# Kernel tuning notes

Measured on AMD Instinct MI355X. Metric: run time of the kernel, lower is better.

The kernel has to match this reference:

```python
import jax, jax.numpy as jnp
import numpy as np

NUM_HEADS = 16

def setup_inputs() -> dict:
    key = jax.random.key(0)
    ks = jax.random.split(key, 6)
    C = 512
    nW, B, N = 64, 4, 144
    x = jax.random.normal(ks[0], (B * nW, N, C), dtype=jnp.float32)
    mask = jax.random.randint(ks[1], (nW, N, N), 0, 2, dtype=jnp.int32)
    Wqkv = jax.random.normal(ks[2], (C, 3 * C), dtype=jnp.float32) * (1.0 / np.sqrt(C))
    bqkv = jnp.zeros((3 * C,), dtype=jnp.float32)
    Wproj = jax.random.normal(ks[3], (C, C), dtype=jnp.float32) * (1.0 / np.sqrt(C))
    bproj = jnp.zeros((C,), dtype=jnp.float32)
    return {"x": x, "mask": mask, "Wqkv": Wqkv, "bqkv": bqkv, "Wproj": Wproj, "bproj": bproj}

def reference(x, mask, Wqkv, bqkv, Wproj, bproj):
    Bn, N, C = x.shape
    H = NUM_HEADS
    D = C // H
    nW = mask.shape[0]
    B = Bn // nW
    scale = 1.0 / jnp.sqrt(jnp.asarray(D, dtype=x.dtype))

    qkv = x @ Wqkv + bqkv                        # (Bn, N, 3C)
    qkv = qkv.reshape(Bn, N, 3, H, D)            # packed order (qkv, H, D)
    qkv = jnp.transpose(qkv, (2, 0, 3, 1, 4))    # (3, Bn, H, N, D)
    q, k, v = qkv[0], qkv[1], qkv[2]

    # split window-batch dim: (B nW) -> B, nW
    q = q.reshape(B, nW, H, N, D)
    k = k.reshape(B, nW, H, N, D)
    v = v.reshape(B, nW, H, N, D)

    attn = jnp.einsum('bwhnd,bwhmd->bwhnm', q, k) * scale
    bias = jnp.where(mask == 0, -jnp.inf, 0.0).astype(x.dtype)  # (nW, N, N)
    attn = attn + bias.reshape(1, nW, 1, N, N)
    attn = jax.nn.softmax(attn, axis=-1)

    out = jnp.einsum('bwhnm,bwhmd->bwhnd', attn, v)   # (B, nW, H, N, D)
    out = jnp.transpose(out, (0, 1, 3, 2, 4)).reshape(Bn, N, C)
    return out @ Wproj + bproj
```

## Files before the change

kernel.cpp:

```cpp
#include <hip/hip_runtime.h>

typedef unsigned short u16;
typedef unsigned int u32;
typedef __attribute__((ext_vector_type(4))) float f32x4;
typedef __attribute__((ext_vector_type(8))) short bf16x8;
typedef __attribute__((ext_vector_type(4))) u32 u32x4;

__device__ __forceinline__ u16 f2bf(float f) {
  union { float f; u32 u; } v; v.f = f;
  u32 r = v.u + 0x7fffu + ((v.u >> 16) & 1u);
  return (u16)(r >> 16);
}

__device__ __forceinline__ u16 f2bf_rne(float f) {
  u32 w;
  asm("v_cvt_pk_bf16_f32 %0, %1, %2" : "=v"(w) : "v"(f), "v"(f));
  return (u16)w;
}

__device__ __forceinline__ void gload_lds16(const u16* g, u16* l) {
  __builtin_amdgcn_global_load_lds((__attribute__((address_space(1))) const void*)g,
                                   (__attribute__((address_space(3))) void*)l,
                                   16, 0, 0);
}

__global__ void __launch_bounds__(256) k_transpose_w(const float* __restrict__ W,
                                                     u16* __restrict__ Wt, int K, int Nc) {
  __shared__ u16 t[64][72];
  const int tid = threadIdx.x;
  const int kb = blockIdx.x * 64, nb = blockIdx.y * 64;
  const int c4 = (tid & 15) * 4;
  const int r0 = tid >> 4;
#pragma unroll
  for (int rr = 0; rr < 4; ++rr) {
    int r = rr * 16 + r0;
    float4 v = *(const float4*)(W + (size_t)(kb + r) * Nc + nb + c4);
    t[r][c4 + 0] = f2bf(v.x);
    t[r][c4 + 1] = f2bf(v.y);
    t[r][c4 + 2] = f2bf(v.z);
    t[r][c4 + 3] = f2bf(v.w);
  }
  __syncthreads();
  const int c8 = (tid & 7) * 8;
  const int rn = tid >> 3;
#pragma unroll
  for (int rr = 0; rr < 2; ++rr) {
    int n = rr * 32 + rn;
    u16 tmp[8];
#pragma unroll
    for (int j = 0; j < 8; ++j) tmp[j] = t[c8 + j][n];
    *(u32x4*)(Wt + (size_t)(nb + n) * K + kb + c8) = *(const u32x4*)tmp;
  }
}

__global__ void k_mask_bits(const int* __restrict__ mask, u32* __restrict__ mtab) {
  int idx = blockIdx.x * blockDim.x + threadIdx.x;
  if (idx >= 64 * 144 * 8) return;
  int wd = idx & 7;
  int r = idx >> 3;
  u32 bits = 0;
  if (wd < 5) {
    int base = r * 144 + wd * 32;
    int nmax = 144 - wd * 32;
    if (nmax > 32) nmax = 32;
    for (int b = 0; b < nmax; ++b) bits |= (mask[base + b] ? 1u : 0u) << b;
  }
  mtab[idx] = bits;
}

template <bool OUT_BF16, bool A_FP32>
__global__ void __launch_bounds__(256, 3) k_gemm(const void* __restrict__ Ap,
                                                 const u16* __restrict__ Bt,
                                                 const float* __restrict__ bias,
                                                 void* __restrict__ D,
                                                 int Nc, int K, int NB) {
  __shared__ u16 As[128 * 68];
  __shared__ u16 Bs[2][128 * 64];
  const int tid = threadIdx.x;
  const int wave = tid >> 6, lane = tid & 63;
  const int wr = wave >> 1, wc = wave & 1;
  const int l15 = lane & 15, g = lane >> 4;
  const int sx = l15 & 7;
  const f32x4 fzero = {0.f, 0.f, 0.f, 0.f};

  const int cpx = gridDim.x >> 3;
  const int swz = (blockIdx.x & 7) * cpx + (blockIdx.x >> 3);
  const int bm = swz / NB, bn = swz % NB;

  const u16* Bb = Bt + (size_t)bn * 128 * K;

  int rr[4], cc[4];
#pragma unroll
  for (int i = 0; i < 4; ++i) {
    int e = i * 256 + tid;
    rr[i] = e >> 3;
    cc[i] = e & 7;
  }

  f32x4 acc[4][4];
#pragma unroll
  for (int m = 0; m < 4; ++m)
#pragma unroll
    for (int n = 0; n < 4; ++n) acc[m][n] = fzero;

  f32x4 areg[8];
  u32x4 aregb[4];

  auto A_LOAD = [&](int ks) {
    if constexpr (A_FP32) {
      const float* Af = (const float*)Ap;
#pragma unroll
      for (int i = 0; i < 4; ++i) {
        const float* p = Af + (size_t)(bm * 128 + rr[i]) * K + ks + cc[i] * 8;
        areg[2 * i] = *(const f32x4*)(p);
        areg[2 * i + 1] = *(const f32x4*)(p + 4);
      }
    } else {
      const u16* Ab = (const u16*)Ap + (size_t)bm * 128 * K;
#pragma unroll
      for (int i = 0; i < 4; ++i)
        aregb[i] = *(const u32x4*)(Ab + (size_t)rr[i] * K + ks + cc[i] * 8);
    }
  };

  auto A_WRITE = [&]() {
#pragma unroll
    for (int i = 0; i < 4; ++i) {
      u32x4 wv;
      if constexpr (A_FP32) {
        u32 w0, w1, w2, w3;
        asm("v_cvt_pk_bf16_f32 %0, %1, %2" : "=v"(w0) : "v"(areg[2 * i][0]), "v"(areg[2 * i][1]));
        asm("v_cvt_pk_bf16_f32 %0, %1, %2" : "=v"(w1) : "v"(areg[2 * i][2]), "v"(areg[2 * i][3]));
        asm("v_cvt_pk_bf16_f32 %0, %1, %2" : "=v"(w2) : "v"(areg[2 * i + 1][0]), "v"(areg[2 * i + 1][1]));
        asm("v_cvt_pk_bf16_f32 %0, %1, %2" : "=v"(w3) : "v"(areg[2 * i + 1][2]), "v"(areg[2 * i + 1][3]));
        wv[0] = w0; wv[1] = w1; wv[2] = w2; wv[3] = w3;
      } else {
        wv = aregb[i];
      }
      *(u32x4*)(&As[rr[i] * 68 + cc[i] * 8]) = wv;
    }
  };

  auto B_STAGE = [&](int buf, int ks) {
#pragma unroll
    for (int i = 0; i < 4; ++i) {
      int cs = cc[i] ^ (rr[i] & 7);
      gload_lds16(Bb + (size_t)rr[i] * K + ks + (cs << 3), &Bs[buf][(i * 256 + tid) * 8]);
    }
  };

  auto COMPUTE = [&](int buf) {
#pragma unroll
    for (int kk = 0; kk < 2; ++kk) {
      bf16x8 a[4], b[4];
#pragma unroll
      for (int m = 0; m < 4; ++m)
        a[m] = *(const bf16x8*)(&As[(wr * 64 + m * 16 + l15) * 68 + (kk * 4 + g) * 8]);
#pragma unroll
      for (int n = 0; n < 4; ++n)
        b[n] = *(const bf16x8*)(&Bs[buf][(wc * 64 + n * 16 + l15) * 64 + (((kk * 4 + g) ^ sx) << 3)]);
#pragma unroll
      for (int m = 0; m < 4; ++m)
#pragma unroll
        for (int n = 0; n < 4; ++n)
          acc[m][n] = __builtin_amdgcn_mfma_f32_16x16x32_bf16(a[m], b[n], acc[m][n], 0, 0, 0);
    }
  };

  const int nt = K >> 6;
  A_LOAD(0);
  B_STAGE(0, 0);
  int cur = 0;
  for (int t = 0; t < nt; ++t) {
    asm volatile("s_waitcnt vmcnt(0)" ::: "memory");
    __builtin_amdgcn_sched_barrier(0);
    if (t + 1 < nt) B_STAGE(cur ^ 1, (t + 1) << 6);
    A_WRITE();
    if (t + 1 < nt) A_LOAD((t + 1) << 6);
    asm volatile("s_waitcnt lgkmcnt(0)" ::: "memory");
    __builtin_amdgcn_sched_barrier(0);
    __builtin_amdgcn_s_barrier();
    __builtin_amdgcn_sched_barrier(0);
    COMPUTE(cur);
    __builtin_amdgcn_sched_barrier(0);
    if (t + 1 < nt) __builtin_amdgcn_s_barrier();
    cur ^= 1;
  }

  const int row0 = bm * 128 + wr * 64;
  const int col0 = bn * 128 + wc * 64;
#pragma unroll
  for (int m = 0; m < 4; ++m) {
#pragma unroll
    for (int n = 0; n < 4; ++n) {
      int col = col0 + n * 16 + l15;
      float bv = bias[col];
#pragma unroll
      for (int j = 0; j < 4; ++j) {
        int row = row0 + m * 16 + g * 4 + j;
        float v = acc[m][n][j] + bv;
        if constexpr (OUT_BF16)
          ((u16*)D)[(size_t)row * Nc + col] = f2bf_rne(v);
        else
          ((float*)D)[(size_t)row * Nc + col] = v;
      }
    }
  }
}

__global__ void __launch_bounds__(192) k_attn(const u16* __restrict__ qkv,
                                              const u32* __restrict__ mtab,
                                              u16* __restrict__ obuf) {
  __shared__ u16 k_s[144 * 40];
  __shared__ u16 vT_s[32 * 168];
  __shared__ u16 P_s[3][16 * 168];

  const int bh = blockIdx.x;
  const int bn = bh >> 4, h = bh & 15;
  const int wid = bn & 63;
  const int tid = threadIdx.x;
  const int wave = tid >> 6, lane = tid & 63;
  const int l15 = lane & 15, g = lane >> 4;
  const f32x4 fzero = {0.f, 0.f, 0.f, 0.f};

  const u16* base = qkv + (size_t)bn * 144 * 1536 + h * 32;
  u16* Pw = &P_s[wave][0];

  bf16x8 qb[3];
  u32 mw[3][5];
#pragma unroll
  for (int it = 0; it < 3; ++it) {
    const int mt = wave + it * 3;
    qb[it] = *(const bf16x8*)(base + (size_t)(mt * 16 + l15) * 1536 + g * 8);
    const u32* mp = mtab + ((size_t)(wid * 144 + mt * 16 + l15) << 3);
#pragma unroll
    for (int wd = 0; wd < 5; ++wd) mw[it][wd] = mp[wd];
  }

  *(u32*)(Pw + l15 * 168 + 144 + g * 4) = 0;
  *(u32*)(Pw + l15 * 168 + 144 + g * 4 + 2) = 0;

  for (int e = tid; e < 576; e += 192) {
    int n = e >> 2, c = e & 3;
    const u16* rowp = base + (size_t)n * 1536 + c * 8;
    u32x4 kv = *(const u32x4*)(rowp + 512);
    u32x4 vv = *(const u32x4*)(rowp + 1024);
    *(u32x4*)(k_s + n * 40 + c * 8) = kv;
#pragma unroll
    for (int t = 0; t < 4; ++t) {
      u32 w = vv[t];
      vT_s[(c * 8 + 2 * t) * 168 + n] = (u16)(w & 0xffffu);
      vT_s[(c * 8 + 2 * t + 1) * 168 + n] = (u16)(w >> 16);
    }
  }
  for (int e = tid; e < 512; e += 192) {
    int d = e >> 4, c = e & 15;
    vT_s[d * 168 + 144 + c] = 0;
  }
  __syncthreads();

  const float scale = 0.17677669529663687f;

#pragma unroll
  for (int it = 0; it < 3; ++it) {
    const int mt = wave + it * 3;

    f32x4 accs[9];
#pragma unroll
    for (int nt = 0; nt < 9; ++nt) {
      bf16x8 kf = *(const bf16x8*)(k_s + (nt * 16 + l15) * 40 + g * 8);
      accs[nt] = __builtin_amdgcn_mfma_f32_16x16x32_bf16(kf, qb[it], fzero, 0, 0, 0);
    }

    float rsum = 0.f;
#pragma unroll
    for (int nt = 0; nt < 9; ++nt) {
      const int wd = nt >> 1;
      const int shb = (nt & 1) * 16;
#pragma unroll
      for (int j = 0; j < 4; ++j) {
        float e = __expf(accs[nt][j] * scale);
        u32 bit = (mw[it][wd] >> (shb + g * 4 + j)) & 1u;
        e = bit ? e : 0.f;
        accs[nt][j] = e;
        rsum += e;
      }
    }
    rsum += __shfl_xor(rsum, 16, 64);
    rsum += __shfl_xor(rsum, 32, 64);
    const float rinv = 1.f / rsum;

#pragma unroll
    for (int nt = 0; nt < 9; ++nt) {
      u32 w0, w1;
      float p0 = accs[nt][0] * rinv, p1 = accs[nt][1] * rinv;
      float p2 = accs[nt][2] * rinv, p3 = accs[nt][3] * rinv;
      asm("v_cvt_pk_bf16_f32 %0, %1, %2" : "=v"(w0) : "v"(p0), "v"(p1));
      asm("v_cvt_pk_bf16_f32 %0, %1, %2" : "=v"(w1) : "v"(p2), "v"(p3));
      *(u32*)(Pw + l15 * 168 + nt * 16 + g * 4) = w0;
      *(u32*)(Pw + l15 * 168 + nt * 16 + g * 4 + 2) = w1;
    }

    asm volatile("s_waitcnt lgkmcnt(0)" ::: "memory");
    __builtin_amdgcn_sched_barrier(0);

    f32x4 acco[2];
    acco[0] = fzero;
    acco[1] = fzero;
#pragma unroll
    for (int kk = 0; kk < 5; ++kk) {
      bf16x8 pa = *(const bf16x8*)(Pw + l15 * 168 + kk * 32 + g * 8);
#pragma unroll
      for (int nt2 = 0; nt2 < 2; ++nt2) {
        bf16x8 b = *(const bf16x8*)(vT_s + (nt2 * 16 + l15) * 168 + kk * 32 + g * 8);
        acco[nt2] = __builtin_amdgcn_mfma_f32_16x16x32_bf16(pa, b, acco[nt2], 0, 0, 0);
      }
    }
#pragma unroll
    for (int nt2 = 0; nt2 < 2; ++nt2)
#pragma unroll
      for (int j = 0; j < 4; ++j) {
        int r = mt * 16 + g * 4 + j;
        int d = nt2 * 16 + l15;
        obuf[((size_t)bn * 144 + r) * 512 + h * 32 + d] = f2bf_rne(acco[nt2][j]);
      }
  }
}

extern "C" void kernel_launch(void* const* d_in, const int* in_sizes, int n_in,
                              void* d_out, int out_size, void* d_ws, size_t ws_size,
                              hipStream_t stream) {
  const float* x = (const float*)d_in[0];
  const int* mask = (const int*)d_in[1];
  const float* Wqkv = (const float*)d_in[2];
  const float* bqkv = (const float*)d_in[3];
  const float* Wproj = (const float*)d_in[4];
  const float* bproj = (const float*)d_in[5];
  float* out = (float*)d_out;

  char* ws = (char*)d_ws;
  u32* mtab    = (u32*)(ws + 0);
  u16* wqkv_t  = (u16*)(ws + 294912);
  u16* qkv     = (u16*)(ws + 1867776);
  u16* obuf    = (u16*)(ws + 115113984);
  u16* wproj_t = (u16*)(ws + 152862720);

  k_transpose_w<<<dim3(8, 24), 256, 0, stream>>>(Wqkv, wqkv_t, 512, 1536);
  k_transpose_w<<<dim3(8, 8), 256, 0, stream>>>(Wproj, wproj_t, 512, 512);
  k_mask_bits<<<288, 256, 0, stream>>>(mask, mtab);
  k_gemm<true, true><<<3456, 256, 0, stream>>>(x, wqkv_t, bqkv, qkv, 1536, 512, 12);
  k_attn<<<4096, 192, 0, stream>>>(qkv, mtab, obuf);
  k_gemm<false, false><<<1152, 256, 0, stream>>>(obuf, wproj_t, bproj, out, 512, 512, 4);
}
```

Measured before the change: 196.9 us.

## Enlarge GEMM tiles to 256 rows, ballot mask packing, pipeline attention softmax

The GEMM kernel moves to 512-thread blocks with 256-row A tiles that share each 128-column B tile, so B traffic per output drops and grid sizes are halved. The mask bit-packing kernel now uses wave ballots instead of serial per-thread loops. The attention kernel software-pipelines QK^T and softmax of the next row tile around the PV MFMAs and raises wave priority during the MFMAs. This costs more LDS and registers per block, which may lower occupancy.

```diff
diff --git a/kernel.cpp b/kernel.cpp
--- a/kernel.cpp
+++ b/kernel.cpp
@@ -2,6 +2,7 @@
 
 typedef unsigned short u16;
 typedef unsigned int u32;
+typedef unsigned long long u64;
 typedef __attribute__((ext_vector_type(4))) float f32x4;
 typedef __attribute__((ext_vector_type(8))) short bf16x8;
 typedef __attribute__((ext_vector_type(4))) u32 u32x4;
@@ -53,28 +54,30 @@
   }
 }
 
-__global__ void k_mask_bits(const int* __restrict__ mask, u32* __restrict__ mtab) {
-  int idx = blockIdx.x * blockDim.x + threadIdx.x;
-  if (idx >= 64 * 144 * 8) return;
-  int wd = idx & 7;
-  int r = idx >> 3;
-  u32 bits = 0;
-  if (wd < 5) {
-    int base = r * 144 + wd * 32;
-    int nmax = 144 - wd * 32;
-    if (nmax > 32) nmax = 32;
-    for (int b = 0; b < nmax; ++b) bits |= (mask[base + b] ? 1u : 0u) << b;
-  }
-  mtab[idx] = bits;
+__global__ void __launch_bounds__(256) k_mask_bits(const int* __restrict__ mask,
+                                                   u32* __restrict__ mtab) {
+  const int row = blockIdx.x * 4 + (threadIdx.x >> 6);
+  const int lane = threadIdx.x & 63;
+  const int* base = mask + (size_t)row * 144;
+  u64 b01 = __ballot(base[lane] != 0);
+  u64 b23 = __ballot(base[64 + lane] != 0);
+  int v4 = (lane < 16) ? base[128 + lane] : 0;
+  u64 b4 = __ballot(v4 != 0);
+  if (lane == 0) {
+    u32* o = mtab + (size_t)row * 8;
+    o[0] = (u32)b01; o[1] = (u32)(b01 >> 32);
+    o[2] = (u32)b23; o[3] = (u32)(b23 >> 32);
+    o[4] = (u32)b4;  o[5] = 0; o[6] = 0; o[7] = 0;
+  }
 }
 
 template <bool OUT_BF16, bool A_FP32>
-__global__ void __launch_bounds__(256, 3) k_gemm(const void* __restrict__ Ap,
+__global__ void __launch_bounds__(512, 2) k_gemm(const void* __restrict__ Ap,
                                                  const u16* __restrict__ Bt,
                                                  const float* __restrict__ bias,
                                                  void* __restrict__ D,
                                                  int Nc, int K, int NB) {
-  __shared__ u16 As[128 * 68];
+  __shared__ u16 As[256 * 68];
   __shared__ u16 Bs[2][128 * 64];
   const int tid = threadIdx.x;
   const int wave = tid >> 6, lane = tid & 63;
@@ -92,7 +95,7 @@
   int rr[4], cc[4];
 #pragma unroll
   for (int i = 0; i < 4; ++i) {
-    int e = i * 256 + tid;
+    int e = i * 512 + tid;
     rr[i] = e >> 3;
     cc[i] = e & 7;
   }
@@ -111,12 +114,12 @@
       const float* Af = (const float*)Ap;
 #pragma unroll
       for (int i = 0; i < 4; ++i) {
-        const float* p = Af + (size_t)(bm * 128 + rr[i]) * K + ks + cc[i] * 8;
+        const float* p = Af + (size_t)(bm * 256 + rr[i]) * K + ks + cc[i] * 8;
         areg[2 * i] = *(const f32x4*)(p);
         areg[2 * i + 1] = *(const f32x4*)(p + 4);
       }
     } else {
-      const u16* Ab = (const u16*)Ap + (size_t)bm * 128 * K;
+      const u16* Ab = (const u16*)Ap + (size_t)bm * 256 * K;
 #pragma unroll
       for (int i = 0; i < 4; ++i)
         aregb[i] = *(const u32x4*)(Ab + (size_t)rr[i] * K + ks + cc[i] * 8);
@@ -143,9 +146,11 @@
 
   auto B_STAGE = [&](int buf, int ks) {
 #pragma unroll
-    for (int i = 0; i < 4; ++i) {
-      int cs = cc[i] ^ (rr[i] & 7);
-      gload_lds16(Bb + (size_t)rr[i] * K + ks + (cs << 3), &Bs[buf][(i * 256 + tid) * 8]);
+    for (int i = 0; i < 2; ++i) {
+      int e = i * 512 + tid;
+      int r = e >> 3, c = e & 7;
+      int cs = c ^ (r & 7);
+      gload_lds16(Bb + (size_t)r * K + ks + (cs << 3), &Bs[buf][e * 8]);
     }
   };
 
@@ -187,7 +192,7 @@
     cur ^= 1;
   }
 
-  const int row0 = bm * 128 + wr * 64;
+  const int row0 = bm * 256 + wr * 64;
   const int col0 = bn * 128 + wc * 64;
 #pragma unroll
   for (int m = 0; m < 4; ++m) {
@@ -261,34 +266,41 @@
 
   const float scale = 0.17677669529663687f;
 
+  f32x4 accs[9];
+  float rinv;
+
+#define QKT(IT)                                                                  \
+  {                                                                              \
+    _Pragma("unroll") for (int nt = 0; nt < 9; ++nt) {                           \
+      bf16x8 kf = *(const bf16x8*)(k_s + (nt * 16 + l15) * 40 + g * 8);          \
+      accs[nt] = __builtin_amdgcn_mfma_f32_16x16x32_bf16(kf, qb[IT], fzero, 0, 0, 0); \
+    }                                                                            \
+  }
+#define SM(IT)                                                                   \
+  {                                                                              \
+    float rsum = 0.f;                                                            \
+    _Pragma("unroll") for (int nt = 0; nt < 9; ++nt) {                           \
+      const int wd = nt >> 1;                                                    \
+      const int shb = (nt & 1) * 16;                                             \
+      _Pragma("unroll") for (int j = 0; j < 4; ++j) {                            \
+        float e = __expf(accs[nt][j] * scale);                                   \
+        u32 bit = (mw[IT][wd] >> (shb + g * 4 + j)) & 1u;                        \
+        e = bit ? e : 0.f;                                                       \
+        accs[nt][j] = e;                                                         \
+        rsum += e;                                                               \
+      }                                                                          \
+    }                                                                            \
+    rsum += __shfl_xor(rsum, 16, 64);                                            \
+    rsum += __shfl_xor(rsum, 32, 64);                                            \
+    rinv = 1.f / rsum;                                                           \
+  }
+
+  QKT(0);
+  SM(0);
+
 #pragma unroll
   for (int it = 0; it < 3; ++it) {
     const int mt = wave + it * 3;
-
-    f32x4 accs[9];
-#pragma unroll
-    for (int nt = 0; nt < 9; ++nt) {
-      bf16x8 kf = *(const bf16x8*)(k_s + (nt * 16 + l15) * 40 + g * 8);
-      accs[nt] = __builtin_amdgcn_mfma_f32_16x16x32_bf16(kf, qb[it], fzero, 0, 0, 0);
-    }
-
-    float rsum = 0.f;
-#pragma unroll
-    for (int nt = 0; nt < 9; ++nt) {
-      const int wd = nt >> 1;
-      const int shb = (nt & 1) * 16;
-#pragma unroll
-      for (int j = 0; j < 4; ++j) {
-        float e = __expf(accs[nt][j] * scale);
-        u32 bit = (mw[it][wd] >> (shb + g * 4 + j)) & 1u;
-        e = bit ? e : 0.f;
-        accs[nt][j] = e;
-        rsum += e;
-      }
-    }
-    rsum += __shfl_xor(rsum, 16, 64);
-    rsum += __shfl_xor(rsum, 32, 64);
-    const float rinv = 1.f / rsum;
 
 #pragma unroll
     for (int nt = 0; nt < 9; ++nt) {
@@ -301,12 +313,16 @@
       *(u32*)(Pw + l15 * 168 + nt * 16 + g * 4 + 2) = w1;
     }
 
+    if (it == 0) QKT(1);
+    if (it == 1) QKT(2);
+
     asm volatile("s_waitcnt lgkmcnt(0)" ::: "memory");
     __builtin_amdgcn_sched_barrier(0);
 
     f32x4 acco[2];
     acco[0] = fzero;
     acco[1] = fzero;
+    __builtin_amdgcn_s_setprio(1);
 #pragma unroll
     for (int kk = 0; kk < 5; ++kk) {
       bf16x8 pa = *(const bf16x8*)(Pw + l15 * 168 + kk * 32 + g * 8);
@@ -316,6 +332,11 @@
         acco[nt2] = __builtin_amdgcn_mfma_f32_16x16x32_bf16(pa, b, acco[nt2], 0, 0, 0);
       }
     }
+    __builtin_amdgcn_s_setprio(0);
+
+    if (it == 0) SM(1);
+    if (it == 1) SM(2);
+
 #pragma unroll
     for (int nt2 = 0; nt2 < 2; ++nt2)
 #pragma unroll
@@ -325,6 +346,8 @@
         obuf[((size_t)bn * 144 + r) * 512 + h * 32 + d] = f2bf_rne(acco[nt2][j]);
       }
   }
+#undef QKT
+#undef SM
 }
 
 extern "C" void kernel_launch(void* const* d_in, const int* in_sizes, int n_in,
@@ -347,8 +370,8 @@
 
   k_transpose_w<<<dim3(8, 24), 256, 0, stream>>>(Wqkv, wqkv_t, 512, 1536);
   k_transpose_w<<<dim3(8, 8), 256, 0, stream>>>(Wproj, wproj_t, 512, 512);
-  k_mask_bits<<<288, 256, 0, stream>>>(mask, mtab);
-  k_gemm<true, true><<<3456, 256, 0, stream>>>(x, wqkv_t, bqkv, qkv, 1536, 512, 12);
+  k_mask_bits<<<2304, 256, 0, stream>>>(mask, mtab);
+  k_gemm<true, true><<<1728, 512, 0, stream>>>(x, wqkv_t, bqkv, qkv, 1536, 512, 12);
   k_attn<<<4096, 192, 0, stream>>>(qkv, mtab, obuf);
-  k_gemm<false, false><<<1152, 256, 0, stream>>>(obuf, wproj_t, bproj, out, 512, 512, 4);
-}
+  k_gemm<false, false><<<576, 512, 0, stream>>>(obuf, wproj_t, bproj, out, 512, 512, 4);
+}
```

After: 229.4 us. 1.17x slower.
